# Optimization experiments

Measured on AMD Instinct MI355X. Metric: run time of the kernel, lower is better.

Reference implementation:

```python
import jax, jax.numpy as jnp
import numpy as np

B, C_IN, C_OUT, H, W = 16, 128, 256, 80, 80
K, STRIDE, PAD = 3, 2, 1
KK = K * K
HO = (H + 2 * PAD - K) // STRIDE + 1
WO = (W + 2 * PAD - K) // STRIDE + 1


def setup_inputs() -> dict:
    key = jax.random.key(0)
    ks = jax.random.split(key, 3)
    x = jax.random.normal(ks[0], (B, C_IN, H, W), jnp.float32)
    offset_w = jax.random.normal(ks[1], (2 * KK, C_IN), jnp.float32) * 0.01
    offset_b = jnp.zeros((2 * KK,), jnp.float32)
    deform_w = jax.random.normal(ks[2], (C_OUT, C_IN, K, K), jnp.float32) * (1.0 / np.sqrt(C_IN * KK))
    deform_b = jnp.zeros((C_OUT,), jnp.float32)
    bn_gamma = jnp.ones((C_OUT,), jnp.float32)
    bn_beta = jnp.zeros((C_OUT,), jnp.float32)
    return dict(x=x, offset_w=offset_w, offset_b=offset_b, deform_w=deform_w,
                deform_b=deform_b, bn_gamma=bn_gamma, bn_beta=bn_beta)


def _bilinear_gather(x, py, px):
    # x: [B,C,H,W]; py,px: [B,KK,HO,WO] float sample coords; zero-pad outside.
    Bb, C, Hh, Ww = x.shape
    y0 = jnp.floor(py)
    x0 = jnp.floor(px)
    wy1 = py - y0
    wx1 = px - x0
    y0i = y0.astype(jnp.int32)
    x0i = x0.astype(jnp.int32)
    flat = x.reshape(Bb, C, Hh * Ww)

    def gather(yi, xi):
        valid = (yi >= 0) & (yi < Hh) & (xi >= 0) & (xi < Ww)
        idx = jnp.clip(yi, 0, Hh - 1) * Ww + jnp.clip(xi, 0, Ww - 1)
        g = jax.vmap(lambda f, i: f[:, i])(flat, idx.reshape(Bb, -1))
        g = g.reshape(Bb, C, *yi.shape[1:])
        return g * valid[:, None].astype(x.dtype)

    g00 = gather(y0i, x0i)
    g01 = gather(y0i, x0i + 1)
    g10 = gather(y0i + 1, x0i)
    g11 = gather(y0i + 1, x0i + 1)
    wy1 = wy1[:, None]  # [B,1,KK,HO,WO]
    wx1 = wx1[:, None]
    wy0 = 1.0 - wy1
    wx0 = 1.0 - wx1
    return wy0 * (wx0 * g00 + wx1 * g01) + wy1 * (wx0 * g10 + wx1 * g11)


def reference(x, offset_w, offset_b, deform_w, deform_b, bn_gamma, bn_beta):
    Bb = x.shape[0]
    # offset conv: 1x1, stride 2 (H,W even -> simple subsample)
    xs = x[:, :, ::2, ::2]  # [B,C,HO,WO]
    off = jnp.einsum('oc,bchw->bohw', offset_w, xs) + offset_b[None, :, None, None]
    off = off.reshape(Bb, KK, 2, HO, WO)  # torchvision layout: (dy,dx) per kernel tap
    dy, dx = off[:, :, 0], off[:, :, 1]
    ky = (jnp.arange(KK) // K).astype(jnp.float32)
    kx = (jnp.arange(KK) % K).astype(jnp.float32)
    base_y = (jnp.arange(HO) * STRIDE - PAD).astype(jnp.float32)
    base_x = (jnp.arange(WO) * STRIDE - PAD).astype(jnp.float32)
    py = base_y[None, None, :, None] + ky[None, :, None, None] + dy
    px = base_x[None, None, None, :] + kx[None, :, None, None] + dx
    sampled = _bilinear_gather(x, py, px)  # [B,C,KK,HO,WO]
    w = deform_w.reshape(C_OUT, C_IN * KK)
    out = jnp.einsum('ok,bkhw->bohw', w, sampled.reshape(Bb, C_IN * KK, HO, WO))
    out = out + deform_b[None, :, None, None]
    # BatchNorm2d in training mode (batch stats, biased var, eps=1e-5)
    mean = out.mean(axis=(0, 2, 3))
    var = out.var(axis=(0, 2, 3))
    out = (out - mean[None, :, None, None]) * jax.lax.rsqrt(var + 1e-5)[None, :, None, None]
    out = out * bn_gamma[None, :, None, None] + bn_beta[None, :, None, None]
    # SiLU
    return out * jax.nn.sigmoid(out)
```

## Files before the change

### kernel.cpp

```cpp
#include <hip/hip_runtime.h>
#include <hip/hip_bf16.h>

#define B_    16
#define CIN_  128
#define COUT_ 256
#define H_    80
#define W_    80
#define HO_   40
#define WO_   40
#define KK_   9
#define SK_   1152
#define NPIX_ 25600
#define NKS_  36

typedef __attribute__((ext_vector_type(8))) short short8;
typedef __attribute__((ext_vector_type(4))) float floatx4;

__device__ __forceinline__ unsigned short f2bu(float v) {
  __hip_bfloat16 h = __float2bfloat16(v);
  return *reinterpret_cast<unsigned short*>(&h);
}
__device__ __forceinline__ float bu2f(unsigned short u) {
  return __uint_as_float(((unsigned)u) << 16);
}
__device__ __forceinline__ unsigned int pk2(float a, float b) {
  return (unsigned)f2bu(a) | ((unsigned)f2bu(b) << 16);
}
__device__ __forceinline__ void gl_lds16(const unsigned short* g, unsigned short* l) {
  __builtin_amdgcn_global_load_lds(
      (const __attribute__((address_space(1))) unsigned int*)(const void*)g,
      (__attribute__((address_space(3))) unsigned int*)(void*)l, 16, 0, 0);
}

__global__ __launch_bounds__(256) void k_pack(const float* __restrict__ dw,
                                              unsigned short* __restrict__ Apk) {
  int t = blockIdx.x * 256 + threadIdx.x;
  int j  = t & 7;
  int sl = (t >> 3) & 3;
  int m  = (t >> 5) & 255;
  int ks = t >> 13;
  int qd = (sl - (m >> 1)) & 3;
  int k  = ks * 32 + qd * 8 + j;
  int kk = k >> 7, ci = k & 127;
  Apk[t] = f2bu(dw[m * SK_ + ci * KK_ + kk]);
}

__global__ __launch_bounds__(256) void k_cl(const float* __restrict__ x,
                                            const float* __restrict__ ow,
                                            const float* __restrict__ ob,
                                            unsigned short* __restrict__ xcl,
                                            float* __restrict__ off) {
  __shared__ unsigned int ts[CIN_ * 41];
  __shared__ float owl[18 * CIN_];
  __shared__ float obl[18];
  const int tid = threadIdx.x;
  const int bid = blockIdx.x;
  const int xcd = bid & 7;
  const int i0_ = bid >> 3;
  const int b   = (i0_ / 80) * 8 + xcd;
  const int y   = i0_ % 80;
  const bool even = (y & 1) == 0;

  for (int j = tid; j < CIN_ * 20; j += 256) {
    int ci = j / 20, xq = j % 20;
    float4 v = *(const float4*)&x[(((size_t)b * CIN_ + ci) * H_ + y) * W_ + xq * 4];
    ts[ci * 41 + xq * 2 + 0] = pk2(v.x, v.y);
    ts[ci * 41 + xq * 2 + 1] = pk2(v.z, v.w);
  }
  if (even) {
    for (int j = tid; j < 18 * CIN_; j += 256) owl[j] = ow[j];
    if (tid < 18) obl[tid] = ob[tid];
  }
  __syncthreads();

  unsigned short* op = xcl + ((size_t)b * H_ * W_ + (size_t)y * W_) * CIN_;
  for (int j = tid; j < 40 * 32; j += 256) {
    int xw = j >> 5, cg = j & 31;
    unsigned w0 = ts[(cg * 4 + 0) * 41 + xw];
    unsigned w1 = ts[(cg * 4 + 1) * 41 + xw];
    unsigned w2 = ts[(cg * 4 + 2) * 41 + xw];
    unsigned w3 = ts[(cg * 4 + 3) * 41 + xw];
    uint2 lo = make_uint2((w0 & 0xFFFFu) | (w1 << 16),
                          (w2 & 0xFFFFu) | (w3 << 16));
    uint2 hi = make_uint2((w0 >> 16) | (w1 & 0xFFFF0000u),
                          (w2 >> 16) | (w3 & 0xFFFF0000u));
    *(uint2*)(op + (size_t)(2 * xw) * CIN_ + cg * 4)     = lo;
    *(uint2*)(op + (size_t)(2 * xw + 1) * CIN_ + cg * 4) = hi;
  }

  if (even) {
    const int ho = y >> 1;
    for (int i = tid; i < 18 * WO_; i += 256) {
      int o = i / WO_, wo = i - o * WO_;
      float acc = obl[o];
      const float* wr = &owl[o * CIN_];
#pragma unroll 4
      for (int ci = 0; ci < CIN_; ci++)
        acc += wr[ci] * bu2f((unsigned short)(ts[ci * 41 + wo] & 0xFFFFu));
      off[((b * 18 + o) * HO_ + ho) * WO_ + wo] = acc;
    }
  }
}

__global__ __launch_bounds__(256) void k_sample_cl(const unsigned short* __restrict__ xcl,
                                                   const float* __restrict__ off,
                                                   unsigned short* __restrict__ Spk) {
  __shared__ __align__(16) int   pidx[80 * 4];
  __shared__ __align__(16) float pw[80 * 4];
  const int tid = threadIdx.x;
  const int j0   = blockIdx.x;
  const int xcd  = j0 & 7;
  const int s    = j0 >> 3;
  const int b_hi = s / 180;
  const int t0   = s % 180;
  const int g    = t0 / 9;
  const int kk   = t0 % 9;
  const int b    = b_hi * 8 + xcd;
  const int ho0  = g * 2;

  if (tid < 80) {
    int hop = tid / 40, px = tid % 40;
    int ho = ho0 + hop;
    float dy = off[((b * 18 + 2 * kk) * HO_ + ho) * WO_ + px];
    float dx = off[((b * 18 + 2 * kk + 1) * HO_ + ho) * WO_ + px];
    float py  = (float)(2 * ho - 1 + (kk / 3)) + dy;
    float pxf = (float)(2 * px - 1 + (kk % 3)) + dx;
    float y0f = floorf(py), x0f = floorf(pxf);
    float wy1 = py - y0f, wx1 = pxf - x0f;
    float wy0 = 1.f - wy1, wx0 = 1.f - wx1;
    int y0 = (int)y0f, x0 = (int)x0f;
    int y1 = y0 + 1, x1 = x0 + 1;
    bool vy0 = (y0 >= 0) && (y0 < H_);
    bool vy1 = (y1 >= 0) && (y1 < H_);
    bool vx0 = (x0 >= 0) && (x0 < W_);
    bool vx1 = (x1 >= 0) && (x1 < W_);
    int y0c = min(max(y0, 0), H_ - 1), y1c = min(max(y1, 0), H_ - 1);
    int x0c = min(max(x0, 0), W_ - 1), x1c = min(max(x1, 0), W_ - 1);
    pidx[tid * 4 + 0] = (y0c * W_ + x0c) << 7;  pw[tid * 4 + 0] = (vy0 && vx0) ? wy0 * wx0 : 0.f;
    pidx[tid * 4 + 1] = (y0c * W_ + x1c) << 7;  pw[tid * 4 + 1] = (vy0 && vx1) ? wy0 * wx1 : 0.f;
    pidx[tid * 4 + 2] = (y1c * W_ + x0c) << 7;  pw[tid * 4 + 2] = (vy1 && vx0) ? wy1 * wx0 : 0.f;
    pidx[tid * 4 + 3] = (y1c * W_ + x1c) << 7;  pw[tid * 4 + 3] = (vy1 && vx1) ? wy1 * wx1 : 0.f;
  }
  __syncthreads();

  const unsigned short* xb = xcl + (size_t)b * (H_ * W_ * CIN_);
#pragma unroll
  for (int it = 0; it < 5; it++) {
    int i = it * 256 + tid;
    int oct = i & 15;
    int pxh = i >> 4;
    int4   I  = *(const int4*)&pidx[pxh * 4];
    float4 Wv = *(const float4*)&pw[pxh * 4];
    short8 c00 = *(const short8*)(xb + I.x + oct * 8);
    short8 c01 = *(const short8*)(xb + I.y + oct * 8);
    short8 c10 = *(const short8*)(xb + I.z + oct * 8);
    short8 c11 = *(const short8*)(xb + I.w + oct * 8);
    short8 r;
#pragma unroll
    for (int i2 = 0; i2 < 8; i2++) {
      float v = Wv.x * bu2f((unsigned short)c00[i2]) +
                Wv.y * bu2f((unsigned short)c01[i2]) +
                Wv.z * bu2f((unsigned short)c10[i2]) +
                Wv.w * bu2f((unsigned short)c11[i2]);
      r[i2] = (short)f2bu(v);
    }
    int p  = b * 1600 + (ho0 + (pxh / 40)) * 40 + (pxh % 40);
    int pt = p >> 4, lm = p & 15;
    int ks = kk * 4 + (oct >> 2);
    int qd = oct & 3;
    *(short8*)&Spk[(((size_t)pt * NKS_ + ks) * 64 + qd * 16 + lm) * 8] = r;
  }
}

__global__ __launch_bounds__(256) void k_gemm(const unsigned short* __restrict__ Apk,
                                              const unsigned short* __restrict__ Spk,
                                              float* __restrict__ out,
                                              float* __restrict__ accum) {
  __shared__ __align__(16) unsigned short a_sh[4][8192];
  __shared__ __align__(16) unsigned short b_sh[4][4096];

  const int tid = threadIdx.x;
  const int wv = tid >> 6;
  const int ln = tid & 63;
  const int lm = ln & 15;
  const int qd = ln >> 4;
  const int wch = wv & 1;
  const int wpx = wv >> 1;

  const int bid = blockIdx.x;
  const int pt0 = bid * 8;

  const unsigned short* ag = Apk + wv * 2048 + ln * 8;
  const unsigned short* bg = Spk + ln * 8;

#define STAGE(t, bf) do {                                                       \
    gl_lds16(ag + (size_t)(t) * 8192 + 0 * 512, &a_sh[bf][wv * 2048 + 0 * 512]);\
    gl_lds16(ag + (size_t)(t) * 8192 + 1 * 512, &a_sh[bf][wv * 2048 + 1 * 512]);\
    gl_lds16(ag + (size_t)(t) * 8192 + 2 * 512, &a_sh[bf][wv * 2048 + 2 * 512]);\
    gl_lds16(ag + (size_t)(t) * 8192 + 3 * 512, &a_sh[bf][wv * 2048 + 3 * 512]);\
    gl_lds16(bg + ((size_t)(pt0 + wv * 2 + 0) * NKS_ + (t)) * 512,              \
             &b_sh[bf][wv * 1024 + 0 * 512]);                                   \
    gl_lds16(bg + ((size_t)(pt0 + wv * 2 + 1) * NKS_ + (t)) * 512,              \
             &b_sh[bf][wv * 1024 + 1 * 512]);                                   \
  } while (0)

  floatx4 acc[8][4];
#pragma unroll
  for (int mt = 0; mt < 8; mt++)
#pragma unroll
    for (int nt = 0; nt < 4; nt++) acc[mt][nt] = (floatx4){0.f, 0.f, 0.f, 0.f};

  const int slot  = (qd + (lm >> 1)) & 3;
  const int abase = (wch * 128 + lm) * 32 + slot * 8;
  const int bbase = (wpx * 4) * 512 + ln * 8;

  STAGE(0, 0);
  STAGE(1, 1);
  STAGE(2, 2);

#pragma unroll 1
  for (int ks = 0; ks < NKS_; ks++) {
    if (ks < NKS_ - 2)       asm volatile("s_waitcnt vmcnt(12)" ::: "memory");
    else if (ks == NKS_ - 2) asm volatile("s_waitcnt vmcnt(6)" ::: "memory");
    else                     asm volatile("s_waitcnt vmcnt(0)" ::: "memory");
    __builtin_amdgcn_s_barrier();
    if (ks + 3 < NKS_) STAGE(ks + 3, (ks + 3) & 3);

    const unsigned short* al = &a_sh[ks & 3][abase];
    const unsigned short* bl = &b_sh[ks & 3][bbase];
    short8 av[8], bv[4];
#pragma unroll
    for (int mt = 0; mt < 8; mt++) av[mt] = *(const short8*)(al + mt * 512);
#pragma unroll
    for (int nt = 0; nt < 4; nt++) bv[nt] = *(const short8*)(bl + nt * 512);
#pragma unroll
    for (int mt = 0; mt < 8; mt++)
#pragma unroll
      for (int nt = 0; nt < 4; nt++)
        acc[mt][nt] = __builtin_amdgcn_mfma_f32_16x16x32_bf16(av[mt], bv[nt],
                                                              acc[mt][nt], 0, 0, 0);
    asm volatile("s_waitcnt lgkmcnt(0)" ::: "memory");
  }
#undef STAGE

  const int cb0 = wch * 128;
#pragma unroll
  for (int nt = 0; nt < 4; nt++) {
    const int pt = pt0 + wpx * 4 + nt;
    const int bb = pt / 100;
    const int rem = (pt - bb * 100) * 16 + lm;
    float* ob = out + (size_t)bb * COUT_ * 1600 + rem;
#pragma unroll
    for (int mt = 0; mt < 8; mt++) {
#pragma unroll
      for (int r = 0; r < 4; r++)
        ob[(size_t)(cb0 + mt * 16 + qd * 4 + r) * 1600] = acc[mt][nt][r];
    }
  }

  __syncthreads();
  float* red = (float*)&a_sh[0][0];
  if (tid < 256) { red[tid] = 0.f; red[256 + tid] = 0.f; }
  __syncthreads();
#pragma unroll
  for (int mt = 0; mt < 8; mt++) {
#pragma unroll
    for (int r = 0; r < 4; r++) {
      float s = acc[mt][0][r] + acc[mt][1][r] + acc[mt][2][r] + acc[mt][3][r];
      float q = acc[mt][0][r] * acc[mt][0][r] + acc[mt][1][r] * acc[mt][1][r] +
                acc[mt][2][r] * acc[mt][2][r] + acc[mt][3][r] * acc[mt][3][r];
#pragma unroll
      for (int d = 1; d < 16; d <<= 1) {
        s += __shfl_xor(s, d, 16);
        q += __shfl_xor(q, d, 16);
      }
      if (lm == 0) {
        int lc = cb0 + mt * 16 + qd * 4 + r;
        atomicAdd(&red[lc], s);
        atomicAdd(&red[256 + lc], q);
      }
    }
  }
  __syncthreads();
  if (tid < 256) {
    atomicAdd(&accum[tid],         red[tid]);
    atomicAdd(&accum[COUT_ + tid], red[256 + tid]);
  }
}

__global__ __launch_bounds__(256) void k_bn(float* __restrict__ io0,
                                            const float* __restrict__ accum,
                                            const float* __restrict__ gamma,
                                            const float* __restrict__ beta) {
  const int t = blockIdx.x * 256 + threadIdx.x;
  const int i0 = t * 4;
  const int c = (i0 / (HO_ * WO_)) % COUT_;
  const float mean = accum[c] * (1.f / NPIX_);
  const float var  = accum[COUT_ + c] * (1.f / NPIX_) - mean * mean;
  const float inv  = rsqrtf(var + 1e-5f);
  const float g  = gamma[c] * inv;
  const float be = beta[c] - mean * g;
  float4 r0 = *(const float4*)(io0 + i0);
  float v[4] = {r0.x, r0.y, r0.z, r0.w};
#pragma unroll
  for (int q = 0; q < 4; q++) {
    float u = v[q] * g + be;
    v[q] = u / (1.f + expf(-u));
  }
  *(float4*)(io0 + i0) = make_float4(v[0], v[1], v[2], v[3]);
}

extern "C" void kernel_launch(void* const* d_in, const int* in_sizes, int n_in,
                              void* d_out, int out_size, void* d_ws, size_t ws_size,
                              hipStream_t stream) {
  const float* x     = (const float*)d_in[0];
  const float* ow    = (const float*)d_in[1];
  const float* ob    = (const float*)d_in[2];
  const float* dw    = (const float*)d_in[3];
  const float* gamma = (const float*)d_in[5];
  const float* beta  = (const float*)d_in[6];
  float* out = (float*)d_out;

  float* off   = (float*)d_ws;
  float* accum = off + B_ * 18 * HO_ * WO_;
  unsigned short* Apk = (unsigned short*)(accum + 2 * COUT_);
  unsigned short* Spk = Apk + (size_t)SK_ * COUT_;
  unsigned short* xcl = Spk + (size_t)NPIX_ * SK_;

  hipMemsetAsync(accum, 0, 2 * COUT_ * sizeof(float), stream);
  k_pack<<<SK_, 256, 0, stream>>>(dw, Apk);
  k_cl<<<B_ * H_, 256, 0, stream>>>(x, ow, ob, xcl, off);
  k_sample_cl<<<B_ * KK_ * 20, 256, 0, stream>>>(xcl, off, Spk);
  k_gemm<<<200, 256, 0, stream>>>(Apk, Spk, out, accum);
  k_bn<<<(NPIX_ * COUT_ / 4 + 255) / 256, 256, 0, stream>>>(
      out, accum, gamma, beta);
}
```

Baseline: 198.2 us.

## Fuse bilinear sampling into the GEMM, dropping the Spk im2col buffer

Merges the deformable sampling kernel into the GEMM. Each block precomputes bilinear indices and weights for 64 pixels times 9 taps in LDS, then gathers and interpolates the B tile on the fly each k-step into a double-buffered LDS slot. This removes the write and re-read of a large bf16 im2col buffer (about 59 MB) and one launch. The accum memset is also folded into k_pack. In exchange the tile width halves (64 pixels per block, 400 blocks), so the weight A tiles are reloaded twice as often, and each k-step now has gather latency on the critical path with only one step of prefetch.

```diff
diff --git a/kernel.cpp b/kernel.cpp
--- a/kernel.cpp
+++ b/kernel.cpp
@@ -33,8 +33,10 @@
 }
 
 __global__ __launch_bounds__(256) void k_pack(const float* __restrict__ dw,
-                                              unsigned short* __restrict__ Apk) {
+                                              unsigned short* __restrict__ Apk,
+                                              float* __restrict__ accum) {
   int t = blockIdx.x * 256 + threadIdx.x;
+  if (t < 2 * COUT_) accum[t] = 0.f;
   int j  = t & 7;
   int sl = (t >> 3) & 3;
   int m  = (t >> 5) & 255;
@@ -102,82 +104,15 @@
   }
 }
 
-__global__ __launch_bounds__(256) void k_sample_cl(const unsigned short* __restrict__ xcl,
-                                                   const float* __restrict__ off,
-                                                   unsigned short* __restrict__ Spk) {
-  __shared__ __align__(16) int   pidx[80 * 4];
-  __shared__ __align__(16) float pw[80 * 4];
-  const int tid = threadIdx.x;
-  const int j0   = blockIdx.x;
-  const int xcd  = j0 & 7;
-  const int s    = j0 >> 3;
-  const int b_hi = s / 180;
-  const int t0   = s % 180;
-  const int g    = t0 / 9;
-  const int kk   = t0 % 9;
-  const int b    = b_hi * 8 + xcd;
-  const int ho0  = g * 2;
-
-  if (tid < 80) {
-    int hop = tid / 40, px = tid % 40;
-    int ho = ho0 + hop;
-    float dy = off[((b * 18 + 2 * kk) * HO_ + ho) * WO_ + px];
-    float dx = off[((b * 18 + 2 * kk + 1) * HO_ + ho) * WO_ + px];
-    float py  = (float)(2 * ho - 1 + (kk / 3)) + dy;
-    float pxf = (float)(2 * px - 1 + (kk % 3)) + dx;
-    float y0f = floorf(py), x0f = floorf(pxf);
-    float wy1 = py - y0f, wx1 = pxf - x0f;
-    float wy0 = 1.f - wy1, wx0 = 1.f - wx1;
-    int y0 = (int)y0f, x0 = (int)x0f;
-    int y1 = y0 + 1, x1 = x0 + 1;
-    bool vy0 = (y0 >= 0) && (y0 < H_);
-    bool vy1 = (y1 >= 0) && (y1 < H_);
-    bool vx0 = (x0 >= 0) && (x0 < W_);
-    bool vx1 = (x1 >= 0) && (x1 < W_);
-    int y0c = min(max(y0, 0), H_ - 1), y1c = min(max(y1, 0), H_ - 1);
-    int x0c = min(max(x0, 0), W_ - 1), x1c = min(max(x1, 0), W_ - 1);
-    pidx[tid * 4 + 0] = (y0c * W_ + x0c) << 7;  pw[tid * 4 + 0] = (vy0 && vx0) ? wy0 * wx0 : 0.f;
-    pidx[tid * 4 + 1] = (y0c * W_ + x1c) << 7;  pw[tid * 4 + 1] = (vy0 && vx1) ? wy0 * wx1 : 0.f;
-    pidx[tid * 4 + 2] = (y1c * W_ + x0c) << 7;  pw[tid * 4 + 2] = (vy1 && vx0) ? wy1 * wx0 : 0.f;
-    pidx[tid * 4 + 3] = (y1c * W_ + x1c) << 7;  pw[tid * 4 + 3] = (vy1 && vx1) ? wy1 * wx1 : 0.f;
-  }
-  __syncthreads();
-
-  const unsigned short* xb = xcl + (size_t)b * (H_ * W_ * CIN_);
-#pragma unroll
-  for (int it = 0; it < 5; it++) {
-    int i = it * 256 + tid;
-    int oct = i & 15;
-    int pxh = i >> 4;
-    int4   I  = *(const int4*)&pidx[pxh * 4];
-    float4 Wv = *(const float4*)&pw[pxh * 4];
-    short8 c00 = *(const short8*)(xb + I.x + oct * 8);
-    short8 c01 = *(const short8*)(xb + I.y + oct * 8);
-    short8 c10 = *(const short8*)(xb + I.z + oct * 8);
-    short8 c11 = *(const short8*)(xb + I.w + oct * 8);
-    short8 r;
-#pragma unroll
-    for (int i2 = 0; i2 < 8; i2++) {
-      float v = Wv.x * bu2f((unsigned short)c00[i2]) +
-                Wv.y * bu2f((unsigned short)c01[i2]) +
-                Wv.z * bu2f((unsigned short)c10[i2]) +
-                Wv.w * bu2f((unsigned short)c11[i2]);
-      r[i2] = (short)f2bu(v);
-    }
-    int p  = b * 1600 + (ho0 + (pxh / 40)) * 40 + (pxh % 40);
-    int pt = p >> 4, lm = p & 15;
-    int ks = kk * 4 + (oct >> 2);
-    int qd = oct & 3;
-    *(short8*)&Spk[(((size_t)pt * NKS_ + ks) * 64 + qd * 16 + lm) * 8] = r;
-  }
-}
-
-__global__ __launch_bounds__(256) void k_gemm(const unsigned short* __restrict__ Apk,
-                                              const unsigned short* __restrict__ Spk,
-                                              float* __restrict__ out,
-                                              float* __restrict__ accum) {
-  __shared__ __align__(16) unsigned short a_sh[4][8192];
-  __shared__ __align__(16) unsigned short b_sh[4][4096];
+__global__ __launch_bounds__(256) void k_fused(const unsigned short* __restrict__ Apk,
+                                               const unsigned short* __restrict__ xcl,
+                                               const float* __restrict__ off,
+                                               float* __restrict__ out,
+                                               float* __restrict__ accum) {
+  __shared__ __align__(16) unsigned short a_sh[3][8192];
+  __shared__ __align__(16) unsigned short b_sh[2][2048];
+  __shared__ __align__(16) int   pidx4[576][4];
+  __shared__ __align__(16) float pw4[576][4];
 
   const int tid = threadIdx.x;
   const int wv = tid >> 6;
@@ -188,73 +123,119 @@
   const int wpx = wv >> 1;
 
   const int bid = blockIdx.x;
-  const int pt0 = bid * 8;
-
-  const unsigned short* ag = Apk + wv * 2048 + ln * 8;
-  const unsigned short* bg = Spk + ln * 8;
-
-#define STAGE(t, bf) do {                                                       \
-    gl_lds16(ag + (size_t)(t) * 8192 + 0 * 512, &a_sh[bf][wv * 2048 + 0 * 512]);\
-    gl_lds16(ag + (size_t)(t) * 8192 + 1 * 512, &a_sh[bf][wv * 2048 + 1 * 512]);\
-    gl_lds16(ag + (size_t)(t) * 8192 + 2 * 512, &a_sh[bf][wv * 2048 + 2 * 512]);\
-    gl_lds16(ag + (size_t)(t) * 8192 + 3 * 512, &a_sh[bf][wv * 2048 + 3 * 512]);\
-    gl_lds16(bg + ((size_t)(pt0 + wv * 2 + 0) * NKS_ + (t)) * 512,              \
-             &b_sh[bf][wv * 1024 + 0 * 512]);                                   \
-    gl_lds16(bg + ((size_t)(pt0 + wv * 2 + 1) * NKS_ + (t)) * 512,              \
-             &b_sh[bf][wv * 1024 + 1 * 512]);                                   \
+  const int xcd = bid & 7;
+  const int T   = bid >> 3;
+  const int b   = xcd + 8 * (T / 25);
+  const int tl  = T % 25;
+
+  for (int j = tid; j < 576; j += 256) {
+    int ipx = j / 9, kk = j - ipx * 9;
+    int g  = tl * 64 + ipx;
+    int ho = g / 40, wo = g - ho * 40;
+    float dy = off[((b * 18 + 2 * kk) * HO_ + ho) * WO_ + wo];
+    float dx = off[((b * 18 + 2 * kk + 1) * HO_ + ho) * WO_ + wo];
+    float py  = (float)(2 * ho - 1 + (kk / 3)) + dy;
+    float pxf = (float)(2 * wo - 1 + (kk % 3)) + dx;
+    float y0f = floorf(py), x0f = floorf(pxf);
+    float wy1 = py - y0f, wx1 = pxf - x0f;
+    float wy0 = 1.f - wy1, wx0 = 1.f - wx1;
+    int y0 = (int)y0f, x0 = (int)x0f;
+    int y1 = y0 + 1, x1 = x0 + 1;
+    bool vy0 = (y0 >= 0) && (y0 < H_), vy1 = (y1 >= 0) && (y1 < H_);
+    bool vx0 = (x0 >= 0) && (x0 < W_), vx1 = (x1 >= 0) && (x1 < W_);
+    int y0c = min(max(y0, 0), H_ - 1), y1c = min(max(y1, 0), H_ - 1);
+    int x0c = min(max(x0, 0), W_ - 1), x1c = min(max(x1, 0), W_ - 1);
+    int base = b * (H_ * W_ * CIN_);
+    pidx4[j][0] = base + (y0c * W_ + x0c) * CIN_;  pw4[j][0] = (vy0 && vx0) ? wy0 * wx0 : 0.f;
+    pidx4[j][1] = base + (y0c * W_ + x1c) * CIN_;  pw4[j][1] = (vy0 && vx1) ? wy0 * wx1 : 0.f;
+    pidx4[j][2] = base + (y1c * W_ + x0c) * CIN_;  pw4[j][2] = (vy1 && vx0) ? wy1 * wx0 : 0.f;
+    pidx4[j][3] = base + (y1c * W_ + x1c) * CIN_;  pw4[j][3] = (vy1 && vx1) ? wy1 * wx1 : 0.f;
+  }
+  __syncthreads();
+
+#define STAGE_A(t, bf) do {                                                    \
+    const unsigned short* s_ = Apk + (size_t)(t) * 8192 + wv * 2048 + ln * 8;  \
+    gl_lds16(s_ + 0 * 512, &a_sh[bf][wv * 2048 + 0 * 512]);                    \
+    gl_lds16(s_ + 1 * 512, &a_sh[bf][wv * 2048 + 1 * 512]);                    \
+    gl_lds16(s_ + 2 * 512, &a_sh[bf][wv * 2048 + 2 * 512]);                    \
+    gl_lds16(s_ + 3 * 512, &a_sh[bf][wv * 2048 + 3 * 512]);                    \
   } while (0)
 
-  floatx4 acc[8][4];
+#define GATHER(t) do {                                                         \
+    int kk_ = (t) >> 2, ci0_ = ((t) & 3) * 32;                                 \
+    int mi_ = ((wv << 4) + lm) * 9 + kk_;                                      \
+    Ig = *(const int4*)&pidx4[mi_][0];                                         \
+    Wg = *(const float4*)&pw4[mi_][0];                                         \
+    int co_ = ci0_ + qd * 8;                                                   \
+    g00 = *(const short8*)(xcl + Ig.x + co_);                                  \
+    g01 = *(const short8*)(xcl + Ig.y + co_);                                  \
+    g10 = *(const short8*)(xcl + Ig.z + co_);                                  \
+    g11 = *(const short8*)(xcl + Ig.w + co_);                                  \
+  } while (0)
+
+  floatx4 acc[8][2];
 #pragma unroll
   for (int mt = 0; mt < 8; mt++)
 #pragma unroll
-    for (int nt = 0; nt < 4; nt++) acc[mt][nt] = (floatx4){0.f, 0.f, 0.f, 0.f};
-
+    for (int nt = 0; nt < 2; nt++) acc[mt][nt] = (floatx4){0.f, 0.f, 0.f, 0.f};
+
+  int4 Ig; float4 Wg; short8 g00, g01, g10, g11;
   const int slot  = (qd + (lm >> 1)) & 3;
   const int abase = (wch * 128 + lm) * 32 + slot * 8;
-  const int bbase = (wpx * 4) * 512 + ln * 8;
-
-  STAGE(0, 0);
-  STAGE(1, 1);
-  STAGE(2, 2);
+  const int bbase = (wpx * 2) * 512 + ln * 8;
+
+  STAGE_A(0, 0);
+  GATHER(0);
+  STAGE_A(1, 1);
 
 #pragma unroll 1
-  for (int ks = 0; ks < NKS_; ks++) {
-    if (ks < NKS_ - 2)       asm volatile("s_waitcnt vmcnt(12)" ::: "memory");
-    else if (ks == NKS_ - 2) asm volatile("s_waitcnt vmcnt(6)" ::: "memory");
-    else                     asm volatile("s_waitcnt vmcnt(0)" ::: "memory");
+  for (int t = 0; t < NKS_; t++) {
+    if (t == NKS_ - 1) asm volatile("s_waitcnt vmcnt(0)" ::: "memory");
+    else               asm volatile("s_waitcnt vmcnt(4)" ::: "memory");
+
+    short8 rb;
+#pragma unroll
+    for (int i2 = 0; i2 < 8; i2++) {
+      float v = Wg.x * bu2f((unsigned short)g00[i2]) +
+                Wg.y * bu2f((unsigned short)g01[i2]) +
+                Wg.z * bu2f((unsigned short)g10[i2]) +
+                Wg.w * bu2f((unsigned short)g11[i2]);
+      rb[i2] = (short)f2bu(v);
+    }
+    *(short8*)&b_sh[t & 1][wv * 512 + ln * 8] = rb;
+    asm volatile("s_waitcnt lgkmcnt(0)" ::: "memory");
     __builtin_amdgcn_s_barrier();
-    if (ks + 3 < NKS_) STAGE(ks + 3, (ks + 3) & 3);
-
-    const unsigned short* al = &a_sh[ks & 3][abase];
-    const unsigned short* bl = &b_sh[ks & 3][bbase];
-    short8 av[8], bv[4];
+
+    if (t + 1 < NKS_) GATHER(t + 1);
+    if (t + 2 < NKS_) STAGE_A(t + 2, (t + 2) % 3);
+
+    const unsigned short* al = &a_sh[t % 3][abase];
+    const unsigned short* bl = &b_sh[t & 1][bbase];
+    short8 av[8], bv[2];
 #pragma unroll
     for (int mt = 0; mt < 8; mt++) av[mt] = *(const short8*)(al + mt * 512);
 #pragma unroll
-    for (int nt = 0; nt < 4; nt++) bv[nt] = *(const short8*)(bl + nt * 512);
+    for (int nt = 0; nt < 2; nt++) bv[nt] = *(const short8*)(bl + nt * 512);
 #pragma unroll
     for (int mt = 0; mt < 8; mt++)
 #pragma unroll
-      for (int nt = 0; nt < 4; nt++)
+      for (int nt = 0; nt < 2; nt++)
         acc[mt][nt] = __builtin_amdgcn_mfma_f32_16x16x32_bf16(av[mt], bv[nt],
                                                               acc[mt][nt], 0, 0, 0);
-    asm volatile("s_waitcnt lgkmcnt(0)" ::: "memory");
-  }
-#undef STAGE
+  }
+#undef STAGE_A
+#undef GATHER
 
   const int cb0 = wch * 128;
-#pragma unroll
-  for (int nt = 0; nt < 4; nt++) {
-    const int pt = pt0 + wpx * 4 + nt;
-    const int bb = pt / 100;
-    const int rem = (pt - bb * 100) * 16 + lm;
-    float* ob = out + (size_t)bb * COUT_ * 1600 + rem;
+  float* ob = out + (size_t)b * COUT_ * 1600;
+#pragma unroll
+  for (int nt = 0; nt < 2; nt++) {
+    const int rem = tl * 64 + (wpx * 2 + nt) * 16 + lm;
 #pragma unroll
     for (int mt = 0; mt < 8; mt++) {
 #pragma unroll
       for (int r = 0; r < 4; r++)
-        ob[(size_t)(cb0 + mt * 16 + qd * 4 + r) * 1600] = acc[mt][nt][r];
+        ob[(size_t)(cb0 + mt * 16 + qd * 4 + r) * 1600 + rem] = acc[mt][nt][r];
     }
   }
 
@@ -266,9 +247,8 @@
   for (int mt = 0; mt < 8; mt++) {
 #pragma unroll
     for (int r = 0; r < 4; r++) {
-      float s = acc[mt][0][r] + acc[mt][1][r] + acc[mt][2][r] + acc[mt][3][r];
-      float q = acc[mt][0][r] * acc[mt][0][r] + acc[mt][1][r] * acc[mt][1][r] +
-                acc[mt][2][r] * acc[mt][2][r] + acc[mt][3][r] * acc[mt][3][r];
+      float s = acc[mt][0][r] + acc[mt][1][r];
+      float q = acc[mt][0][r] * acc[mt][0][r] + acc[mt][1][r] * acc[mt][1][r];
 #pragma unroll
       for (int d = 1; d < 16; d <<= 1) {
         s += __shfl_xor(s, d, 16);
@@ -324,14 +304,11 @@
   float* off   = (float*)d_ws;
   float* accum = off + B_ * 18 * HO_ * WO_;
   unsigned short* Apk = (unsigned short*)(accum + 2 * COUT_);
-  unsigned short* Spk = Apk + (size_t)SK_ * COUT_;
-  unsigned short* xcl = Spk + (size_t)NPIX_ * SK_;
-
-  hipMemsetAsync(accum, 0, 2 * COUT_ * sizeof(float), stream);
-  k_pack<<<SK_, 256, 0, stream>>>(dw, Apk);
+  unsigned short* xcl = Apk + (size_t)SK_ * COUT_;
+
+  k_pack<<<SK_, 256, 0, stream>>>(dw, Apk, accum);
   k_cl<<<B_ * H_, 256, 0, stream>>>(x, ow, ob, xcl, off);
-  k_sample_cl<<<B_ * KK_ * 20, 256, 0, stream>>>(xcl, off, Spk);
-  k_gemm<<<200, 256, 0, stream>>>(Apk, Spk, out, accum);
+  k_fused<<<400, 256, 0, stream>>>(Apk, xcl, off, out, accum);
   k_bn<<<(NPIX_ * COUT_ / 4 + 255) / 256, 256, 0, stream>>>(
       out, accum, gamma, beta);
 }
```

Result: faster. 192.2 us (-3.0%).
